# Kernel tuning notes

Measured on AMD Instinct MI355X. Metric: run time of the kernel, lower is better.

Reference implementation:

```python
import jax, jax.numpy as jnp
import numpy as np

HEADS = 16
DIM_HEAD = 64

def setup_inputs() -> dict:
    key = jax.random.key(0)
    ks = jax.random.split(key, 5)
    B, S, D = 2, 2048, 1024
    return {
        "hidden_states": jax.random.normal(ks[0], (B, S, D), dtype=jnp.float32),
        "Wq": jax.random.normal(ks[1], (D, D), dtype=jnp.float32) * (D ** -0.5),
        "Wkv": jax.random.normal(ks[2], (D, D), dtype=jnp.float32) * (D ** -0.5),
        "Wout": jax.random.normal(ks[3], (D, D), dtype=jnp.float32) * (D ** -0.5),
        "bout": jnp.zeros((D,), dtype=jnp.float32),
    }

def reference(hidden_states, Wq, Wkv, Wout, bout):
    B, S, D = hidden_states.shape
    H, Dh = HEADS, DIM_HEAD
    # projections (torch Linear: x @ W.T; here weights are stored as [in, out])
    q = hidden_states @ Wq            # [B, S, D]
    kv = hidden_states @ Wkv          # key == value share the to_kv projection
    q = q.reshape(B, S, H, Dh).transpose(0, 2, 1, 3)   # [B, H, S, Dh]
    k = kv.reshape(B, S, H, Dh).transpose(0, 2, 1, 3)
    v = k
    scale = 1.0 / np.sqrt(Dh).astype(np.float32)
    # ReLU attention: no softmax
    attn = jax.nn.relu(jnp.einsum("bhsd,bhtd->bhst", q, k) * scale)  # [B,H,S,S]
    out = jnp.einsum("bhst,bhtd->bhsd", attn, v)                     # [B,H,S,Dh]
    out = out.transpose(0, 2, 1, 3).reshape(B, S, H * Dh)
    return out @ Wout + bout
```

## Files before the change

kernel.cpp:

```cpp
#include <hip/hip_runtime.h>
#include <hip/hip_bf16.h>

#define HEADS  16
#define DIMH   64
#define NBATCH 2
#define SEQ    2048
#define DMODEL 1024
#define MROWS  (NBATCH * SEQ)

typedef __attribute__((ext_vector_type(8)))  short bf16x8;
typedef __attribute__((ext_vector_type(4)))  float f32x4;
typedef __attribute__((ext_vector_type(16))) float f32x16;
typedef __attribute__((ext_vector_type(4)))  float float4v;
typedef __attribute__((ext_vector_type(4)))  short short4v;
typedef __attribute__((ext_vector_type(8)))  short short8v;

__device__ inline void glds16(const void* g, void* l) {
    __builtin_amdgcn_global_load_lds(
        (const __attribute__((address_space(1))) unsigned int*)g,
        (__attribute__((address_space(3))) unsigned int*)l, 16, 0, 0);
}

#define WAIT_VMCNT(N) asm volatile("s_waitcnt vmcnt(" #N ")" ::: "memory")
#define BARRIER() do { __builtin_amdgcn_s_barrier(); asm volatile("" ::: "memory"); } while (0)

__global__ void prep_kernel(const float* __restrict__ hs,
                            const float* __restrict__ Wq,
                            const float* __restrict__ Wkv,
                            const float* __restrict__ Wout,
                            __hip_bfloat16* __restrict__ hsb,
                            __hip_bfloat16* __restrict__ WqT,
                            __hip_bfloat16* __restrict__ WkvT,
                            __hip_bfloat16* __restrict__ WoT) {
    __shared__ float tile[64][65];
    const int tid = threadIdx.x;
    const int bid = blockIdx.x;
    if (bid < 768) {
        const int w = bid >> 8;
        const int tnum = bid & 255;
        const int bx = tnum & 15;
        const int by = tnum >> 4;
        const float* __restrict__ W = (w == 0) ? Wq : (w == 1) ? Wkv : Wout;
        __hip_bfloat16* __restrict__ WT = (w == 0) ? WqT : (w == 1) ? WkvT : WoT;
        const int ty = tid >> 6, tx = tid & 63;
#pragma unroll
        for (int r = 0; r < 16; ++r)
            tile[ty * 16 + r][tx] = W[(size_t)(by * 64 + ty * 16 + r) * DMODEL + bx * 64 + tx];
        __syncthreads();
#pragma unroll
        for (int r = 0; r < 16; ++r)
            WT[(size_t)(bx * 64 + ty * 16 + r) * DMODEL + by * 64 + tx] =
                __float2bfloat16(tile[tx][ty * 16 + r]);
    } else {
        const int cb = bid - 768;
#pragma unroll
        for (int jj = 0; jj < 4; ++jj) {
            int i = cb * 1024 + jj * 256 + tid;
            float4v v = reinterpret_cast<const float4v*>(hs)[i];
            union { short4v s; __hip_bfloat16 h[4]; } u;
#pragma unroll
            for (int j = 0; j < 4; ++j) u.h[j] = __float2bfloat16(v[j]);
            reinterpret_cast<short4v*>(hsb)[i] = u.s;
        }
    }
}

__global__ void combine_kernel(const __hip_bfloat16* __restrict__ p0,
                               const __hip_bfloat16* __restrict__ p1,
                               __hip_bfloat16* __restrict__ out, int n8) {
    int i = blockIdx.x * blockDim.x + threadIdx.x;
    if (i >= n8) return;
    union { short8v s; __hip_bfloat16 h[8]; } a, b, u;
    a.s = reinterpret_cast<const short8v*>(p0)[i];
    b.s = reinterpret_cast<const short8v*>(p1)[i];
#pragma unroll
    for (int j = 0; j < 8; ++j)
        u.h[j] = __float2bfloat16(__bfloat162float(a.h[j]) + __bfloat162float(b.h[j]));
    reinterpret_cast<short8v*>(out)[i] = u.s;
}

__launch_bounds__(512, 4)
__global__ void proj_kernel(const __hip_bfloat16* __restrict__ hsb,
                            const __hip_bfloat16* __restrict__ WqT,
                            const __hip_bfloat16* __restrict__ WkvT,
                            __hip_bfloat16* __restrict__ qb,
                            __hip_bfloat16* __restrict__ kb,
                            __hip_bfloat16* __restrict__ vtb) {
    __shared__ __align__(16) char SLDS[49152];
    char (*Alds)[8192] = (char (*)[8192])SLDS;
    char (*Blds)[8192] = (char (*)[8192])(SLDS + 24576);
    char* CT = SLDS;

    const int tid  = threadIdx.x;
    const int wave = tid >> 6;
    const int lane = tid & 63;
    const int lr = lane & 15;
    const int lk = lane >> 4;
    const int wm = wave >> 1, wn = wave & 1;

    int bid = blockIdx.x;
    bid = (bid & 7) * 64 + (bid >> 3);
    const int xt = bid & 15;
    const int mt = bid >> 4;
    const bool is_q = xt < 8;
    const int mbase = mt * 128;
    const int nbase = (xt & 7) * 128;
    const __hip_bfloat16* __restrict__ WT = is_q ? WqT : WkvT;

    const char* __restrict__ Ab = (const char*)(hsb + (size_t)mbase * DMODEL);
    const char* __restrict__ Bb = (const char*)(WT + (size_t)nbase * DMODEL);

    auto stage = [&](int buf, int k0) {
        const size_t colb = (size_t)k0 * 2 + lk * 16;
        const size_t rowoff = (size_t)(wave * 16 + lr) * (DMODEL * 2);
        glds16(Ab + rowoff + colb, &Alds[buf][wave * 1024]);
        glds16(Bb + rowoff + colb, &Blds[buf][wave * 1024]);
    };

    stage(0, 0);
    stage(1, 32);

    f32x4 acc[2][4] = {};
    int c0 = 0;
    for (int t = 0; t < DMODEL / 32; ++t) {
        if (t < DMODEL / 32 - 1) WAIT_VMCNT(2); else WAIT_VMCNT(0);
        BARRIER();
        if (t + 2 < DMODEL / 32) {
            int sb = c0 + 2; if (sb >= 3) sb -= 3;
            stage(sb, (t + 2) * 32);
        }
        bf16x8 af[2], bfr[4];
#pragma unroll
        for (int i = 0; i < 2; ++i)
            af[i] = *reinterpret_cast<const bf16x8*>(&Alds[c0][(wm * 2 + i) * 1024 + lane * 16]);
#pragma unroll
        for (int j = 0; j < 4; ++j)
            bfr[j] = *reinterpret_cast<const bf16x8*>(&Blds[c0][(wn * 4 + j) * 1024 + lane * 16]);
#pragma unroll
        for (int i = 0; i < 2; ++i)
#pragma unroll
            for (int j = 0; j < 4; ++j)
                acc[i][j] = __builtin_amdgcn_mfma_f32_16x16x32_bf16(af[i], bfr[j], acc[i][j], 0, 0, 0);
        c0 = (c0 + 1 == 3) ? 0 : c0 + 1;
    }

    const float qscale = is_q ? 0.125f : 1.0f;
    const int b_ = mbase >> 11;
    const int s0 = mbase & (SEQ - 1);
    const int h0 = nbase >> 6;
    BARRIER();

#pragma unroll
    for (int i = 0; i < 2; ++i)
#pragma unroll
        for (int j = 0; j < 4; ++j)
#pragma unroll
            for (int r = 0; r < 4; ++r) {
                int m = wm * 32 + i * 16 + lk * 4 + r;
                int n = wn * 64 + j * 16 + lr;
                *reinterpret_cast<__hip_bfloat16*>(
                    &CT[m * 256 + ((n * 2) ^ (((m >> 2) & 7) << 4))]) =
                    __float2bfloat16(acc[i][j][r] * qscale);
            }
    BARRIER();

    __hip_bfloat16* __restrict__ dst0 = is_q ? qb : kb;
#pragma unroll
    for (int p = 0; p < 4; ++p) {
        int g = p * 64 + (tid >> 3);
        int m = g >> 1, hseg = g & 1, o = tid & 7;
        int key = ((m >> 2) & 7) << 4;
        bf16x8 val = *reinterpret_cast<const bf16x8*>(
            &CT[m * 256 + ((hseg * 128 + o * 16) ^ key)]);
        *reinterpret_cast<bf16x8*>(
            &dst0[(((size_t)b_ * HEADS + h0 + hseg) * SEQ + s0 + m) * DIMH + o * 8]) = val;
    }

    if (!is_q) {
        BARRIER();
#pragma unroll
        for (int i = 0; i < 2; ++i)
#pragma unroll
            for (int j = 0; j < 4; ++j)
#pragma unroll
                for (int r = 0; r < 4; ++r) {
                    int m = wm * 32 + i * 16 + lk * 4 + r;
                    int n = wn * 64 + j * 16 + lr;
                    *reinterpret_cast<__hip_bfloat16*>(
                        &CT[n * 256 + ((m * 2) ^ ((n & 7) << 4))]) =
                        __float2bfloat16(acc[i][j][r]);
                }
        BARRIER();
#pragma unroll
        for (int p = 0; p < 4; ++p) {
            int g = p * 64 + (tid >> 3);
            int n = g >> 1, half = g & 1, o = tid & 7;
            int key2 = (n & 7) << 4;
            int D = half * 64 + o * 8;
            int mm = D >> 4, H = o & 1;
            union { unsigned long long d[2]; bf16x8 v; } val;
            val.d[0] = *reinterpret_cast<const unsigned long long*>(
                &CT[n * 256 + ((mm * 32 + H * 8) ^ key2)]);
            val.d[1] = *reinterpret_cast<const unsigned long long*>(
                &CT[n * 256 + ((mm * 32 + 16 + H * 8) ^ key2)]);
            int h = h0 + (n >> 6);
            int dh = n & 63;
            *reinterpret_cast<bf16x8*>(
                &vtb[(((size_t)b_ * HEADS + h) * DIMH + dh) * SEQ + s0 + D]) = val.v;
        }
    }
}

__launch_bounds__(512, 2)
__global__ void outproj_kernel(const __hip_bfloat16* __restrict__ ao,
                               const __hip_bfloat16* __restrict__ WoT,
                               const float* __restrict__ bout,
                               float* __restrict__ out) {
    __shared__ __align__(16) char Alds[3][8192];
    __shared__ __align__(16) char Blds[3][8192];
    const int tid  = threadIdx.x;
    const int wave = tid >> 6;
    const int lane = tid & 63;
    const int lr = lane & 15;
    const int lk = lane >> 4;
    const int wm = wave >> 1, wn = wave & 1;

    int bid = blockIdx.x;
    bid = (bid & 7) * 32 + (bid >> 3);
    const int xt = bid & 7;
    const int mt = bid >> 3;
    const int mbase = mt * 128;
    const int nbase = xt * 128;

    const char* __restrict__ Ab = (const char*)(ao + (size_t)mbase * DMODEL);
    const char* __restrict__ Bb = (const char*)(WoT + (size_t)nbase * DMODEL);

    auto stage = [&](int buf, int k0) {
        const size_t colb = (size_t)k0 * 2 + lk * 16;
        glds16(Ab + (size_t)(wave * 16 + lr) * (DMODEL * 2) + colb,
               &Alds[buf][wave * 1024]);
        glds16(Bb + (size_t)(wave * 16 + lr) * (DMODEL * 2) + colb,
               &Blds[buf][wave * 1024]);
    };

    stage(0, 0);
    stage(1, 32);

    f32x4 acc[2][4] = {};
    int c0 = 0;
    for (int t = 0; t < DMODEL / 32; ++t) {
        if (t < DMODEL / 32 - 1) WAIT_VMCNT(2); else WAIT_VMCNT(0);
        BARRIER();
        if (t + 2 < DMODEL / 32) {
            int sb = c0 + 2; if (sb >= 3) sb -= 3;
            stage(sb, (t + 2) * 32);
        }
        bf16x8 af[2], bfr[4];
#pragma unroll
        for (int i = 0; i < 2; ++i)
            af[i] = *reinterpret_cast<const bf16x8*>(&Alds[c0][(wm * 2 + i) * 1024 + lane * 16]);
#pragma unroll
        for (int j = 0; j < 4; ++j)
            bfr[j] = *reinterpret_cast<const bf16x8*>(&Blds[c0][(wn * 4 + j) * 1024 + lane * 16]);
#pragma unroll
        for (int i = 0; i < 2; ++i)
#pragma unroll
            for (int j = 0; j < 4; ++j)
                acc[i][j] = __builtin_amdgcn_mfma_f32_16x16x32_bf16(af[i], bfr[j], acc[i][j], 0, 0, 0);
        c0 = (c0 + 1 == 3) ? 0 : c0 + 1;
    }

#pragma unroll
    for (int j = 0; j < 4; ++j) {
        const int n = nbase + wn * 64 + j * 16 + lr;
        const float bias = bout[n];
#pragma unroll
        for (int i = 0; i < 2; ++i) {
#pragma unroll
            for (int r = 0; r < 4; ++r) {
                int m = mbase + wm * 32 + i * 16 + lk * 4 + r;
                out[(size_t)m * DMODEL + n] = acc[i][j][r] + bias;
            }
        }
    }
}

__launch_bounds__(512, 2)
__global__ void attn_kernel(const __hip_bfloat16* __restrict__ qb,
                            const __hip_bfloat16* __restrict__ kb,
                            const __hip_bfloat16* __restrict__ vtb,
                            __hip_bfloat16* __restrict__ po) {
    __shared__ __align__(16) char Klds[4][8192];
    __shared__ __align__(16) char Vlds[4][8192];
    const int lane = threadIdx.x & 63;
    const int wave = threadIdx.x >> 6;
    const int l32  = lane & 31;
    const int hi   = lane >> 5;

    int bid = blockIdx.x;
    bid = (bid & 7) * 32 + (bid >> 3);
    const int ts   = bid & 1;
    const int qblk = (bid >> 1) & 3;
    const int bh   = bid >> 3;
    const int b_ = bh >> 4, h = bh & 15;
    const int qbase = qblk * 512 + wave * 64;
    const int tbeg = ts * (SEQ / 2);

    const __hip_bfloat16* __restrict__ Q = qb + (size_t)bh * SEQ * DIMH;
    const char* __restrict__ Kg = (const char*)(kb  + (size_t)bh * SEQ * DIMH);
    const char* __restrict__ Vg = (const char*)(vtb + (size_t)bh * DIMH * SEQ);

    bf16x8 qf[2][4];
#pragma unroll
    for (int g = 0; g < 2; ++g)
#pragma unroll
        for (int ks = 0; ks < 4; ++ks)
            qf[g][ks] = *reinterpret_cast<const bf16x8*>(
                &Q[(size_t)(qbase + g * 32 + l32) * DIMH + ks * 16 + hi * 8]);

    auto stage = [&](int buf, int t0) {
        glds16(Kg + (size_t)(t0 + (wave >> 2) * 32 + (lane & 31)) * 128 +
                   (wave & 3) * 32 + (lane >> 5) * 16,
               &Klds[buf][wave * 1024]);
        glds16(Vg + (size_t)((wave & 1) * 32 + (lane & 31)) * (SEQ * 2) +
                   (size_t)(t0 + (wave >> 1) * 16) * 2 + (lane >> 5) * 16,
               &Vlds[buf][wave * 1024]);
    };

    f32x16 acco[2][2] = {};

    auto compute = [&](const char* Kc, const char* Vc) {
        f32x16 sp[2][2] = {};
        __builtin_amdgcn_s_setprio(1);
#pragma unroll
        for (int ks = 0; ks < 4; ++ks) {
            bf16x8 k0f = *reinterpret_cast<const bf16x8*>(Kc + ks * 1024 + lane * 16);
            bf16x8 k1f = *reinterpret_cast<const bf16x8*>(Kc + (4 + ks) * 1024 + lane * 16);
            sp[0][0] = __builtin_amdgcn_mfma_f32_32x32x16_bf16(k0f, qf[0][ks], sp[0][0], 0, 0, 0);
            sp[0][1] = __builtin_amdgcn_mfma_f32_32x32x16_bf16(k1f, qf[0][ks], sp[0][1], 0, 0, 0);
            sp[1][0] = __builtin_amdgcn_mfma_f32_32x32x16_bf16(k0f, qf[1][ks], sp[1][0], 0, 0, 0);
            sp[1][1] = __builtin_amdgcn_mfma_f32_32x32x16_bf16(k1f, qf[1][ks], sp[1][1], 0, 0, 0);
        }
#pragma unroll
        for (int kt = 0; kt < 4; ++kt) {
            bf16x8 v0 = *reinterpret_cast<const bf16x8*>(Vc + (kt * 2 + 0) * 1024 + lane * 16);
            bf16x8 v1 = *reinterpret_cast<const bf16x8*>(Vc + (kt * 2 + 1) * 1024 + lane * 16);
            const int rb = (kt & 1) * 8;
#pragma unroll
            for (int g = 0; g < 2; ++g) {
                union { __hip_bfloat16 hh[8]; bf16x8 v; } pa;
#pragma unroll
                for (int j = 0; j < 8; ++j) {
                    float x = (kt < 2) ? sp[g][0][rb + j] : sp[g][1][rb + j];
                    pa.hh[j] = __float2bfloat16(fmaxf(x, 0.f));
                }
                acco[g][0] = __builtin_amdgcn_mfma_f32_32x32x16_bf16(pa.v, v0, acco[g][0], 0, 0, 0);
                acco[g][1] = __builtin_amdgcn_mfma_f32_32x32x16_bf16(pa.v, v1, acco[g][1], 0, 0, 0);
            }
        }
        __builtin_amdgcn_s_setprio(0);
    };

    const int NT = SEQ / 2 / 64;
    stage(0, tbeg);
    stage(1, tbeg + 64);

    for (int t = 0; t < NT; ++t) {
        if (t < NT - 1) WAIT_VMCNT(2); else WAIT_VMCNT(0);
        BARRIER();
        if (t + 2 < NT) stage((t + 2) & 3, tbeg + (t + 2) * 64);
        compute(Klds[t & 3], Vlds[t & 3]);
    }

    __hip_bfloat16* __restrict__ PO = po + (size_t)ts * MROWS * DMODEL;
#pragma unroll
    for (int g = 0; g < 2; ++g)
#pragma unroll
        for (int nt = 0; nt < 2; ++nt)
#pragma unroll
            for (int r = 0; r < 16; ++r) {
                int q = qbase + g * 32 + (r & 3) + 8 * (r >> 2) + 4 * hi;
                PO[(size_t)(b_ * SEQ + q) * DMODEL + h * 64 + nt * 32 + l32] =
                    __float2bfloat16(acco[g][nt][r]);
            }
}

extern "C" void kernel_launch(void* const* d_in, const int* in_sizes, int n_in,
                              void* d_out, int out_size, void* d_ws, size_t ws_size,
                              hipStream_t stream) {
    const float* hs   = (const float*)d_in[0];
    const float* Wq   = (const float*)d_in[1];
    const float* Wkv  = (const float*)d_in[2];
    const float* Wout = (const float*)d_in[3];
    const float* bout = (const float*)d_in[4];
    float* out = (float*)d_out;

    char* ws = (char*)d_ws;
    size_t off = 0;
    auto alloc = [&](size_t bytes) { char* p = ws + off; off += bytes; return p; };
    __hip_bfloat16* hsb  = (__hip_bfloat16*)alloc((size_t)MROWS * DMODEL * 2);
    __hip_bfloat16* WqT  = (__hip_bfloat16*)alloc((size_t)DMODEL * DMODEL * 2);
    __hip_bfloat16* WkvT = (__hip_bfloat16*)alloc((size_t)DMODEL * DMODEL * 2);
    __hip_bfloat16* WoT  = (__hip_bfloat16*)alloc((size_t)DMODEL * DMODEL * 2);
    __hip_bfloat16* qb   = (__hip_bfloat16*)alloc((size_t)MROWS * DMODEL * 2);
    __hip_bfloat16* kb   = (__hip_bfloat16*)alloc((size_t)MROWS * DMODEL * 2);
    __hip_bfloat16* vtb  = (__hip_bfloat16*)alloc((size_t)MROWS * DMODEL * 2);
    __hip_bfloat16* po   = (__hip_bfloat16*)alloc((size_t)2 * MROWS * DMODEL * 2);
    __hip_bfloat16* ao   = hsb;

    prep_kernel<<<1792, 256, 0, stream>>>(hs, Wq, Wkv, Wout, hsb, WqT, WkvT, WoT);

    proj_kernel<<<512, 512, 0, stream>>>(hsb, WqT, WkvT, qb, kb, vtb);

    attn_kernel<<<256, 512, 0, stream>>>(qb, kb, vtb, po);

    combine_kernel<<<(MROWS * DMODEL / 8 + 255) / 256, 256, 0, stream>>>(
        po, po + (size_t)MROWS * DMODEL, ao, MROWS * DMODEL / 8);

    outproj_kernel<<<256, 512, 0, stream>>>(ao, WoT, bout, out);
}
```

Before: 114.1 us.

## Stage 128-key tiles per barrier with triple-buffered LDS in attention

The attention loop now stages 128 keys per iteration (two 64-key sub-tiles) into three 32KB LDS buffers instead of 64 keys into four 16KB buffers, and computes both sub-tiles between barriers. This halves the number of barriers and vmcnt waits per block. In exchange the staging footprint grows from 64KB to 96KB of LDS, which may limit how many blocks fit per CU alongside the 512-thread, 2-block launch bound.

```diff
diff --git a/kernel.cpp b/kernel.cpp
--- a/kernel.cpp
+++ b/kernel.cpp
@@ -290,8 +290,8 @@
                             const __hip_bfloat16* __restrict__ kb,
                             const __hip_bfloat16* __restrict__ vtb,
                             __hip_bfloat16* __restrict__ po) {
-    __shared__ __align__(16) char Klds[4][8192];
-    __shared__ __align__(16) char Vlds[4][8192];
+    __shared__ __align__(16) char Klds[3][16384];
+    __shared__ __align__(16) char Vlds[3][16384];
     const int lane = threadIdx.x & 63;
     const int wave = threadIdx.x >> 6;
     const int l32  = lane & 31;
@@ -319,23 +319,26 @@
                 &Q[(size_t)(qbase + g * 32 + l32) * DIMH + ks * 16 + hi * 8]);
 
     auto stage = [&](int buf, int t0) {
-        glds16(Kg + (size_t)(t0 + (wave >> 2) * 32 + (lane & 31)) * 128 +
-                   (wave & 3) * 32 + (lane >> 5) * 16,
-               &Klds[buf][wave * 1024]);
-        glds16(Vg + (size_t)((wave & 1) * 32 + (lane & 31)) * (SEQ * 2) +
-                   (size_t)(t0 + (wave >> 1) * 16) * 2 + (lane >> 5) * 16,
-               &Vlds[buf][wave * 1024]);
+        const int krow = (wave >> 2) * 32 + l32;
+        const int kcol = (wave & 3) * 32 + hi * 16;
+        glds16(Kg + (size_t)(t0 + krow) * 128 + kcol,       &Klds[buf][wave * 1024]);
+        glds16(Kg + (size_t)(t0 + 64 + krow) * 128 + kcol,  &Klds[buf][(8 + wave) * 1024]);
+        const size_t vrow = (size_t)((wave & 1) * 32 + l32) * (SEQ * 2);
+        const int vcol = (wave >> 1) * 32 + hi * 16;
+        glds16(Vg + vrow + (size_t)t0 * 2 + vcol,           &Vlds[buf][wave * 1024]);
+        glds16(Vg + vrow + (size_t)(t0 + 64) * 2 + vcol,    &Vlds[buf][(8 + wave) * 1024]);
     };
 
     f32x16 acco[2][2] = {};
 
-    auto compute = [&](const char* Kc, const char* Vc) {
+    auto compute = [&](const char* Kc, const char* Vc, int u) {
+        const int ro = u * 8192;
         f32x16 sp[2][2] = {};
         __builtin_amdgcn_s_setprio(1);
 #pragma unroll
         for (int ks = 0; ks < 4; ++ks) {
-            bf16x8 k0f = *reinterpret_cast<const bf16x8*>(Kc + ks * 1024 + lane * 16);
-            bf16x8 k1f = *reinterpret_cast<const bf16x8*>(Kc + (4 + ks) * 1024 + lane * 16);
+            bf16x8 k0f = *reinterpret_cast<const bf16x8*>(Kc + ro + ks * 1024 + lane * 16);
+            bf16x8 k1f = *reinterpret_cast<const bf16x8*>(Kc + ro + (4 + ks) * 1024 + lane * 16);
             sp[0][0] = __builtin_amdgcn_mfma_f32_32x32x16_bf16(k0f, qf[0][ks], sp[0][0], 0, 0, 0);
             sp[0][1] = __builtin_amdgcn_mfma_f32_32x32x16_bf16(k1f, qf[0][ks], sp[0][1], 0, 0, 0);
             sp[1][0] = __builtin_amdgcn_mfma_f32_32x32x16_bf16(k0f, qf[1][ks], sp[1][0], 0, 0, 0);
@@ -343,8 +346,8 @@
         }
 #pragma unroll
         for (int kt = 0; kt < 4; ++kt) {
-            bf16x8 v0 = *reinterpret_cast<const bf16x8*>(Vc + (kt * 2 + 0) * 1024 + lane * 16);
-            bf16x8 v1 = *reinterpret_cast<const bf16x8*>(Vc + (kt * 2 + 1) * 1024 + lane * 16);
+            bf16x8 v0 = *reinterpret_cast<const bf16x8*>(Vc + ro + (kt * 2 + 0) * 1024 + lane * 16);
+            bf16x8 v1 = *reinterpret_cast<const bf16x8*>(Vc + ro + (kt * 2 + 1) * 1024 + lane * 16);
             const int rb = (kt & 1) * 8;
 #pragma unroll
             for (int g = 0; g < 2; ++g) {
@@ -361,15 +364,20 @@
         __builtin_amdgcn_s_setprio(0);
     };
 
-    const int NT = SEQ / 2 / 64;
+    const int NT = SEQ / 2 / 128;
     stage(0, tbeg);
-    stage(1, tbeg + 64);
+    stage(1, tbeg + 128);
 
     for (int t = 0; t < NT; ++t) {
-        if (t < NT - 1) WAIT_VMCNT(2); else WAIT_VMCNT(0);
+        if (t < NT - 1) WAIT_VMCNT(4); else WAIT_VMCNT(0);
         BARRIER();
-        if (t + 2 < NT) stage((t + 2) & 3, tbeg + (t + 2) * 64);
-        compute(Klds[t & 3], Vlds[t & 3]);
+        if (t + 2 < NT) {
+            int sb = t + 2; sb -= (sb / 3) * 3;
+            stage(sb, tbeg + (t + 2) * 128);
+        }
+        const int c0 = t % 3;
+        compute(Klds[c0], Vlds[c0], 0);
+        compute(Klds[c0], Vlds[c0], 1);
     }
 
     __hip_bfloat16* __restrict__ PO = po + (size_t)ts * MROWS * DMODEL;
```

After: 113.4 us. About the same (-0.7%).
